# Kernel tuning notes

Measured on AMD Instinct MI355X. Metric: run time of the kernel, lower is better.

## Reference

```python
import jax, jax.numpy as jnp
import numpy as np

B = 32768

def _lin(x, w, b):
    return x @ w.T + b

def setup_inputs() -> dict:
    key = jax.random.key(0)
    ks = iter(jax.random.split(key, 40))
    def rn(shape, s=0.05):
        return jax.random.normal(next(ks), shape, dtype=jnp.float32) * s
    inp = {
        'img_feat': jax.random.normal(next(ks), (B, 256), dtype=jnp.float32),
        'instruction_idx': jax.random.randint(next(ks), (B, 1), 0, 4),
        '_hx': jax.random.normal(next(ks), (B, 256), dtype=jnp.float32),
        '_cx': jax.random.normal(next(ks), (B, 256), dtype=jnp.float32),
        'query': jax.random.normal(next(ks), (B, 256), dtype=jnp.float32),
        # parameters
        'emb': rn((4, 25), 1.0),
        'w_ta': rn((256, 25)), 'b_ta': rn((256,)),
        'w_ih': rn((1024, 512)), 'w_hh': rn((1024, 256)),
        'b_ih': rn((1024,)), 'b_hh': rn((1024,)),
        'w_q': rn((256, 256)), 'b_q': rn((256,)),
        'w_k': rn((256, 256)), 'b_k': rn((256,)),
        'w_ba': rn((512, 512)), 'b_ba': rn((512,)),
        'w_at': rn((256, 512)), 'b_at': rn((256,)),
        'w_p1': rn((128, 256)), 'b_p1': rn((128,)),
        'w_p2': rn((64, 128)), 'b_p2': rn((64,)),
        'w_p': rn((3, 64)), 'b_p': rn((3,)),
        'w_v1': rn((64, 256)), 'b_v1': rn((64,)),
        'w_v2': rn((32, 64)), 'b_v2': rn((32,)),
        'w_v': rn((1, 32)), 'b_v': rn((1,)),
    }
    return inp

def reference(img_feat, instruction_idx, _hx, _cx, query,
              emb, w_ta, b_ta, w_ih, w_hh, b_ih, b_hh,
              w_q, b_q, w_k, b_k, w_ba, b_ba, w_at, b_at,
              w_p1, b_p1, w_p2, b_p2, w_p, b_p,
              w_v1, b_v1, w_v2, b_v2, w_v, b_v):
    # embedding lookup [B,1,25] -> [B,25]
    we = emb[instruction_idx].reshape(instruction_idx.shape[0], -1)
    gated_att = jax.nn.sigmoid(_lin(we, w_ta, b_ta))          # [B,256]
    gated_fusion = img_feat * gated_att                        # [B,256]
    lstm_input = jnp.concatenate([gated_fusion, gated_att], 1) # [B,512]
    # LSTMCell (PyTorch gate order: i, f, g, o)
    gates = lstm_input @ w_ih.T + b_ih + _hx @ w_hh.T + b_hh   # [B,1024]
    i, f, g, o = jnp.split(gates, 4, axis=1)
    cx = jax.nn.sigmoid(f) * _cx + jax.nn.sigmoid(i) * jnp.tanh(g)
    hx = jax.nn.sigmoid(o) * jnp.tanh(cx)
    mlp_input = jnp.concatenate([gated_fusion, hx], 1)         # [B,512]
    mlp_attn = jax.nn.relu(_lin(mlp_input, w_ba, b_ba))        # [B,512]
    key_, val = jnp.split(mlp_attn, 2, axis=1)                 # [B,256] each
    w_q_out = jax.nn.relu(_lin(query, w_q, b_q))
    w_k_out = jax.nn.relu(_lin(key_, w_k, b_k))
    u_t = jnp.tanh(w_q_out + w_k_out)
    attention_vector = u_t * val
    attn_weight = jnp.concatenate([attention_vector, hx], 1)   # [B,512]
    attn_weight = jax.nn.relu(_lin(attn_weight, w_at, b_at))   # [B,256]
    pol = jax.nn.relu(_lin(attn_weight, w_p1, b_p1))
    pol = jax.nn.relu(_lin(pol, w_p2, b_p2))
    valh = jax.nn.relu(_lin(attn_weight, w_v1, b_v1))
    valh = jax.nn.relu(_lin(valh, w_v2, b_v2))
    return (_lin(valh, w_v, b_v), _lin(pol, w_p, b_p), hx, cx)
```

## Files before the change

### kernel.cpp

```cpp
#include <hip/hip_runtime.h>

typedef unsigned short u16;
typedef __bf16 bf16x8 __attribute__((ext_vector_type(8)));
typedef float f32x4 __attribute__((ext_vector_type(4)));
typedef u16 u16x8 __attribute__((ext_vector_type(8)));

#define TM 64
#define LDP 264
#define BTOT 32768

#define OFF_WIH 0
#define OFF_WHH 524288
#define OFF_WQ  786432
#define OFF_WK  851968
#define OFF_WBA 917504
#define OFF_WAT 1179648
#define OFF_WP1 1310720
#define OFF_WP2 1343488
#define OFF_WV1 1351680
#define OFF_WV2 1368064

__device__ __forceinline__ float b2f(u16 h) {
    union { unsigned int u; float f; } v; v.u = ((unsigned int)h) << 16; return v.f;
}
__device__ __forceinline__ u16 f2b(float f) {
    union { float f; unsigned int u; } v; v.f = f;
    unsigned int u = v.u + 0x7fffu + ((v.u >> 16) & 1u);
    return (u16)(u >> 16);
}
__device__ __forceinline__ float sigm(float x) { return 1.0f / (1.0f + __expf(-x)); }
__device__ __forceinline__ float tanhfast(float x) { return 1.0f - 2.0f / (__expf(2.0f * x) + 1.0f); }
__device__ __forceinline__ float relu(float x) { return x > 0.0f ? x : 0.0f; }
__device__ __forceinline__ bf16x8 ld8(const u16* p) { return *(const bf16x8*)p; }
__device__ __forceinline__ f32x4 mfma16(bf16x8 a, bf16x8 b, f32x4 c) {
    return __builtin_amdgcn_mfma_f32_16x16x32_bf16(a, b, c, 0, 0, 0);
}

__device__ __forceinline__ bool detect_f32(const void* imgp) {
    const unsigned int* w = (const unsigned int*)imgp;
    int hits = 0;
    #pragma unroll
    for (int i = 0; i < 16; ++i) {
        int e0 = (w[i] >> 7) & 0xFF;
        hits += (e0 >= 100 && e0 <= 140) ? 1 : 0;
    }
    return hits < 10;
}

__device__ __forceinline__ float ldin(const void* p, size_t i, bool f32) {
    return f32 ? ((const float*)p)[i] : b2f(((const u16*)p)[i]);
}
__device__ __forceinline__ void stout(void* o, size_t i, float v, bool f32) {
    if (f32) ((float*)o)[i] = v; else ((u16*)o)[i] = f2b(v);
}
__device__ __forceinline__ float ldin_nt(const void* p, size_t i, bool f32) {
    return f32 ? __builtin_nontemporal_load((const float*)p + i)
               : b2f(((const u16*)p)[i]);
}
__device__ __forceinline__ void stout_nt(void* o, size_t i, float v, bool f32) {
    if (f32) __builtin_nontemporal_store(v, (float*)o + i);
    else ((u16*)o)[i] = f2b(v);
}
__device__ __forceinline__ bf16x8 ldg8f_nt(const void* p, size_t i, bool f32) {
    u16 t[8];
    if (f32) {
        const f32x4* q = (const f32x4*)((const float*)p + i);
        f32x4 a = __builtin_nontemporal_load(q);
        f32x4 b = __builtin_nontemporal_load(q + 1);
        #pragma unroll
        for (int j = 0; j < 4; ++j) { t[j] = f2b(a[j]); t[4 + j] = f2b(b[j]); }
    } else {
        *(u16x8*)t = *(const u16x8*)((const u16*)p + i);
    }
    return *(bf16x8*)t;
}

struct CvtArgs {
    const void* src[10];
    unsigned int nchunk[10];
    unsigned int off8[10];
    unsigned int Kdim[10];
    const void* det;
};

__global__ __launch_bounds__(256) void cvt_weights(CvtArgs a, u16* ws) {
    const bool f32 = detect_f32(a.det);
    const int p = blockIdx.x;
    const void* s = a.src[p];
    const unsigned int K = a.Kdim[p];
    const unsigned int KK = K >> 5;
    const unsigned int msk = KK - 1u;
    const unsigned int sh = 31 - __clz((int)KK);
    const unsigned int n = a.nchunk[p];
    for (unsigned int g = blockIdx.y * blockDim.x + threadIdx.x; g < n;
         g += gridDim.y * blockDim.x) {
        const unsigned int lane = g & 63u;
        const unsigned int fi = g >> 6;
        const unsigned int kk = fi & msk;
        const unsigned int tn = fi >> sh;
        const unsigned int row = tn * 16u + (lane & 15u);
        const unsigned int col = kk * 32u + ((lane >> 4) << 3);
        const size_t si = (size_t)row * K + col;
        u16 t[8];
        if (f32) {
            const float* q = (const float*)s + si;
            #pragma unroll
            for (int j = 0; j < 8; ++j) t[j] = f2b(__builtin_nontemporal_load(q + j));
        } else {
            *(u16x8*)t = *(const u16x8*)((const u16*)s + si);
        }
        ((u16x8*)ws)[a.off8[p] + g] = *(u16x8*)t;
    }
}

__global__ __launch_bounds__(1024, 2) void ac_fused(
    const void* __restrict__ img, const int* __restrict__ insn,
    const void* __restrict__ hx_in, const void* __restrict__ cx_in,
    const void* __restrict__ query,
    const void* __restrict__ emb, const void* __restrict__ w_ta, const void* __restrict__ b_ta,
    const void* __restrict__ b_ih, const void* __restrict__ b_hh,
    const void* __restrict__ b_q, const void* __restrict__ b_k,
    const void* __restrict__ b_ba, const void* __restrict__ b_at,
    const void* __restrict__ b_p1, const void* __restrict__ b_p2,
    const void* __restrict__ w_p3, const void* __restrict__ b_p3,
    const void* __restrict__ b_v1, const void* __restrict__ b_v2,
    const void* __restrict__ w_v3, const void* __restrict__ b_v3,
    const u16* __restrict__ wsb, void* __restrict__ out)
{
    __shared__ __align__(16) u16 sGF[TM * LDP];
    __shared__ __align__(16) u16 sHX0[TM * LDP];
    __shared__ __align__(16) u16 sHX1[TM * LDP];
    __shared__ __align__(16) u16 sKEY[TM * LDP];
    __shared__ __align__(16) u16 sG[4 * LDP];
    __shared__ int sIDX[TM];

    const bool isf32 = detect_f32(img);
    const int tid  = threadIdx.x;
    const int lane = tid & 63;
    const int wv   = tid >> 6;
    const int l15  = lane & 15;
    const int quad = lane >> 4;
    const int q8   = quad * 8;
    const int ln8  = lane * 8;
    const int row0 = blockIdx.x * TM;

    if (tid < TM) sIDX[tid] = insn[row0 + tid];
    {
        int e = tid >> 8, n = tid & 255;
        float acc = ldin(b_ta, n, isf32);
        #pragma unroll
        for (int k = 0; k < 25; ++k)
            acc += ldin(emb, e * 25 + k, isf32) * ldin(w_ta, n * 25 + k, isf32);
        sG[e * LDP + n] = f2b(sigm(acc));
    }
    __syncthreads();

    for (int it = tid; it < TM * 32; it += 1024) {
        int r = it >> 5, c0 = (it & 31) << 3;
        int e = sIDX[r];
        u16x8 gv = *(const u16x8*)(sG + e * LDP + c0);
        float iv[8], hv[8];
        const size_t base = (size_t)(row0 + r) * 256 + c0;
        if (isf32) {
            const f32x4* ip = (const f32x4*)((const float*)img + base);
            const f32x4* hp = (const f32x4*)((const float*)hx_in + base);
            f32x4 a0 = __builtin_nontemporal_load(ip);
            f32x4 a1 = __builtin_nontemporal_load(ip + 1);
            f32x4 b0 = __builtin_nontemporal_load(hp);
            f32x4 b1 = __builtin_nontemporal_load(hp + 1);
            #pragma unroll
            for (int j = 0; j < 4; ++j) {
                iv[j] = a0[j]; iv[4 + j] = a1[j];
                hv[j] = b0[j]; hv[4 + j] = b1[j];
            }
        } else {
            u16x8 i8 = *(const u16x8*)((const u16*)img + base);
            u16x8 h8 = *(const u16x8*)((const u16*)hx_in + base);
            #pragma unroll
            for (int j = 0; j < 8; ++j) { iv[j] = b2f(i8[j]); hv[j] = b2f(h8[j]); }
        }
        u16x8 ov, hvv;
        #pragma unroll
        for (int j = 0; j < 8; ++j) {
            ov[j] = f2b(iv[j] * b2f(gv[j]));
            hvv[j] = f2b(hv[j]);
        }
        *(u16x8*)(sGF + r * LDP + c0) = ov;
        *(u16x8*)(sHX0 + r * LDP + c0) = hvv;
    }
    __syncthreads();

    {
        int eIdx[4];
        #pragma unroll
        for (int m = 0; m < 4; ++m) eIdx[m] = sIDX[m * 16 + l15];
        const u16* bih0 = wsb + OFF_WIH + ln8;
        const u16* bhh0 = wsb + OFF_WHH + ln8;
        const int c = wv;
        f32x4 acc[4][4] = {};
        #pragma unroll
        for (int kk = 0; kk < 8; ++kk) {
            bf16x8 a[4], b[4];
            #pragma unroll
            for (int m = 0; m < 4; ++m) a[m] = ld8(sGF + (m * 16 + l15) * LDP + kk * 32 + q8);
            #pragma unroll
            for (int g = 0; g < 4; ++g) b[g] = ld8(bih0 + (size_t)((g * 16 + c) * 16 + kk) * 512);
            #pragma unroll
            for (int g = 0; g < 4; ++g)
                #pragma unroll
                for (int m = 0; m < 4; ++m) acc[g][m] = mfma16(a[m], b[g], acc[g][m]);
        }
        #pragma unroll
        for (int kk = 0; kk < 8; ++kk) {
            bf16x8 a[4], b[4];
            #pragma unroll
            for (int m = 0; m < 4; ++m) a[m] = ld8(sG + eIdx[m] * LDP + kk * 32 + q8);
            #pragma unroll
            for (int g = 0; g < 4; ++g) b[g] = ld8(bih0 + (size_t)((g * 16 + c) * 16 + 8 + kk) * 512);
            #pragma unroll
            for (int g = 0; g < 4; ++g)
                #pragma unroll
                for (int m = 0; m < 4; ++m) acc[g][m] = mfma16(a[m], b[g], acc[g][m]);
        }
        #pragma unroll
        for (int kk = 0; kk < 8; ++kk) {
            bf16x8 a[4], b[4];
            #pragma unroll
            for (int m = 0; m < 4; ++m) a[m] = ld8(sHX0 + (m * 16 + l15) * LDP + kk * 32 + q8);
            #pragma unroll
            for (int g = 0; g < 4; ++g) b[g] = ld8(bhh0 + (size_t)((g * 16 + c) * 8 + kk) * 512);
            #pragma unroll
            for (int g = 0; g < 4; ++g)
                #pragma unroll
                for (int m = 0; m < 4; ++m) acc[g][m] = mfma16(a[m], b[g], acc[g][m]);
        }
        const int nc = c * 16 + l15;
        const float bi  = ldin(b_ih, nc, isf32)       + ldin(b_hh, nc, isf32);
        const float bff = ldin(b_ih, 256 + nc, isf32) + ldin(b_hh, 256 + nc, isf32);
        const float bg  = ldin(b_ih, 512 + nc, isf32) + ldin(b_hh, 512 + nc, isf32);
        const float bo  = ldin(b_ih, 768 + nc, isf32) + ldin(b_hh, 768 + nc, isf32);
        #pragma unroll
        for (int m = 0; m < 4; ++m) {
            #pragma unroll
            for (int r = 0; r < 4; ++r) {
                const int grow = m * 16 + quad * 4 + r;
                const size_t gidx = (size_t)(row0 + grow) * 256 + nc;
                const float cxo = ldin_nt(cx_in, gidx, isf32);
                const float iv = sigm(acc[0][m][r] + bi);
                const float fv = sigm(acc[1][m][r] + bff);
                const float gv = tanhfast(acc[2][m][r] + bg);
                const float ov = sigm(acc[3][m][r] + bo);
                const float cn = fv * cxo + iv * gv;
                const float hn = ov * tanhfast(cn);
                stout_nt(out, (size_t)(4 * BTOT) + gidx, hn, isf32);
                stout_nt(out, (size_t)(4 * BTOT) + (size_t)256 * BTOT + gidx, cn, isf32);
                sHX1[grow * LDP + nc] = f2b(hn);
            }
        }
    }
    __syncthreads();

    {
        f32x4 acc[2][4] = {};
        const u16* bb0 = wsb + OFF_WBA + ln8;
        #pragma unroll
        for (int kk = 0; kk < 8; ++kk) {
            bf16x8 a[4], b[2];
            #pragma unroll
            for (int m = 0; m < 4; ++m) a[m] = ld8(sGF + (m * 16 + l15) * LDP + kk * 32 + q8);
            #pragma unroll
            for (int t = 0; t < 2; ++t) b[t] = ld8(bb0 + (size_t)((wv * 2 + t) * 16 + kk) * 512);
            #pragma unroll
            for (int t = 0; t < 2; ++t)
                #pragma unroll
                for (int m = 0; m < 4; ++m) acc[t][m] = mfma16(a[m], b[t], acc[t][m]);
        }
        #pragma unroll
        for (int kk = 0; kk < 8; ++kk) {
            bf16x8 a[4], b[2];
            #pragma unroll
            for (int m = 0; m < 4; ++m) a[m] = ld8(sHX1 + (m * 16 + l15) * LDP + kk * 32 + q8);
            #pragma unroll
            for (int t = 0; t < 2; ++t) b[t] = ld8(bb0 + (size_t)((wv * 2 + t) * 16 + 8 + kk) * 512);
            #pragma unroll
            for (int t = 0; t < 2; ++t)
                #pragma unroll
                for (int m = 0; m < 4; ++m) acc[t][m] = mfma16(a[m], b[t], acc[t][m]);
        }
        #pragma unroll
        for (int t = 0; t < 2; ++t) {
            const int col = (wv * 2 + t) * 16 + l15;
            const float bb = ldin(b_ba, col, isf32);
            u16* dst = (col < 256) ? (sKEY + col) : (sHX0 + (col - 256));
            #pragma unroll
            for (int m = 0; m < 4; ++m)
                #pragma unroll
                for (int r = 0; r < 4; ++r)
                    dst[(m * 16 + quad * 4 + r) * LDP] = f2b(relu(acc[t][m][r] + bb));
        }
    }
    __syncthreads();

    {
        f32x4 cq[4] = {}, ck[4] = {};
        const u16* bq0 = wsb + OFF_WQ + ln8;
        const u16* bk0 = wsb + OFF_WK + ln8;
        #pragma unroll
        for (int kk = 0; kk < 8; ++kk) {
            bf16x8 aq[4], ak[4], bqf, bkf;
            #pragma unroll
            for (int m = 0; m < 4; ++m) {
                aq[m] = ldg8f_nt(query, (size_t)(row0 + m * 16 + l15) * 256 + kk * 32 + q8, isf32);
                ak[m] = ld8(sKEY + (m * 16 + l15) * LDP + kk * 32 + q8);
            }
            bqf = ld8(bq0 + (size_t)(wv * 8 + kk) * 512);
            bkf = ld8(bk0 + (size_t)(wv * 8 + kk) * 512);
            #pragma unroll
            for (int m = 0; m < 4; ++m) {
                cq[m] = mfma16(aq[m], bqf, cq[m]);
                ck[m] = mfma16(ak[m], bkf, ck[m]);
            }
        }
        const int col = wv * 16 + l15;
        const float bqv = ldin(b_q, col, isf32);
        const float bkv = ldin(b_k, col, isf32);
        #pragma unroll
        for (int m = 0; m < 4; ++m)
            #pragma unroll
            for (int r = 0; r < 4; ++r) {
                const int grow = m * 16 + quad * 4 + r;
                const float u = tanhfast(relu(cq[m][r] + bqv) + relu(ck[m][r] + bkv));
                sGF[grow * LDP + col] = f2b(u * b2f(sHX0[grow * LDP + col]));
            }
    }
    __syncthreads();

    {
        f32x4 acc[4] = {};
        const u16* bb0 = wsb + OFF_WAT + ln8;
        #pragma unroll
        for (int kk = 0; kk < 8; ++kk) {
            bf16x8 a[4], b;
            #pragma unroll
            for (int m = 0; m < 4; ++m) a[m] = ld8(sGF + (m * 16 + l15) * LDP + kk * 32 + q8);
            b = ld8(bb0 + (size_t)(wv * 16 + kk) * 512);
            #pragma unroll
            for (int m = 0; m < 4; ++m) acc[m] = mfma16(a[m], b, acc[m]);
        }
        #pragma unroll
        for (int kk = 0; kk < 8; ++kk) {
            bf16x8 a[4], b;
            #pragma unroll
            for (int m = 0; m < 4; ++m) a[m] = ld8(sHX1 + (m * 16 + l15) * LDP + kk * 32 + q8);
            b = ld8(bb0 + (size_t)(wv * 16 + 8 + kk) * 512);
            #pragma unroll
            for (int m = 0; m < 4; ++m) acc[m] = mfma16(a[m], b, acc[m]);
        }
        const int col = wv * 16 + l15;
        const float bb = ldin(b_at, col, isf32);
        #pragma unroll
        for (int m = 0; m < 4; ++m)
            #pragma unroll
            for (int r = 0; r < 4; ++r)
                sKEY[(m * 16 + quad * 4 + r) * LDP + col] = f2b(relu(acc[m][r] + bb));
    }
    __syncthreads();

    {
        const int m = wv & 3, half = wv >> 2;
        const int arow = m * 16 + l15;
        bf16x8 afr[8];
        #pragma unroll
        for (int kk = 0; kk < 8; ++kk) afr[kk] = ld8(sKEY + arow * LDP + kk * 32 + q8);
        {
            f32x4 acc[2] = {};
            #pragma unroll
            for (int kk = 0; kk < 8; ++kk)
                #pragma unroll
                for (int t = 0; t < 2; ++t)
                    acc[t] = mfma16(afr[kk], ld8(wsb + OFF_WP1 + (size_t)((half * 2 + t) * 8 + kk) * 512 + ln8), acc[t]);
            #pragma unroll
            for (int t = 0; t < 2; ++t) {
                const int col = (half * 2 + t) * 16 + l15;
                const float bb = ldin(b_p1, col, isf32);
                #pragma unroll
                for (int r = 0; r < 4; ++r)
                    sHX0[(m * 16 + quad * 4 + r) * LDP + col] = f2b(relu(acc[t][r] + bb));
            }
        }
        {
            f32x4 acc = {};
            #pragma unroll
            for (int kk = 0; kk < 8; ++kk)
                acc = mfma16(afr[kk], ld8(wsb + OFF_WV1 + (size_t)(half * 8 + kk) * 512 + ln8), acc);
            const int col = half * 16 + l15;
            const float bb = ldin(b_v1, col, isf32);
            #pragma unroll
            for (int r = 0; r < 4; ++r)
                sHX0[(m * 16 + quad * 4 + r) * LDP + 128 + col] = f2b(relu(acc[r] + bb));
        }
    }
    __syncthreads();

    {
        const int m = wv & 3, half = wv >> 2;
        const int arow = m * 16 + l15;
        const u16* a0 = sHX0 + arow * LDP;
        bf16x8 ap[4], av2[2];
        #pragma unroll
        for (int kk = 0; kk < 4; ++kk) ap[kk] = ld8(a0 + kk * 32 + q8);
        #pragma unroll
        for (int kk = 0; kk < 2; ++kk) av2[kk] = ld8(a0 + 128 + kk * 32 + q8);
        {
            f32x4 acc = {};
            #pragma unroll
            for (int kk = 0; kk < 4; ++kk)
                acc = mfma16(ap[kk], ld8(wsb + OFF_WP2 + (size_t)(half * 4 + kk) * 512 + ln8), acc);
            const int col = half * 16 + l15;
            const float bb = ldin(b_p2, col, isf32);
            #pragma unroll
            for (int r = 0; r < 4; ++r)
                sGF[(m * 16 + quad * 4 + r) * LDP + col] = f2b(relu(acc[r] + bb));
        }
        if (half < 2) {
            f32x4 acc = {};
            #pragma unroll
            for (int kk = 0; kk < 2; ++kk)
                acc = mfma16(av2[kk], ld8(wsb + OFF_WV2 + (size_t)(half * 2 + kk) * 512 + ln8), acc);
            const int col = half * 16 + l15;
            const float bb = ldin(b_v2, col, isf32);
            #pragma unroll
            for (int r = 0; r < 4; ++r)
                sGF[(m * 16 + quad * 4 + r) * LDP + 64 + col] = f2b(relu(acc[r] + bb));
        }
    }
    __syncthreads();

    if (tid < TM * 4) {
        const int r = tid >> 2, o = tid & 3;
        const int grow = row0 + r;
        const u16* rowp = sGF + r * LDP;
        if (o < 3) {
            float acc = ldin(b_p3, o, isf32);
            #pragma unroll
            for (int k = 0; k < 64; ++k) acc += b2f(rowp[k]) * ldin(w_p3, o * 64 + k, isf32);
            stout_nt(out, (size_t)BTOT + (size_t)grow * 3 + o, acc, isf32);
        } else {
            float acc = ldin(b_v3, 0, isf32);
            #pragma unroll
            for (int k = 0; k < 32; ++k) acc += b2f(rowp[64 + k]) * ldin(w_v3, k, isf32);
            stout_nt(out, (size_t)grow, acc, isf32);
        }
    }
}

extern "C" void kernel_launch(void* const* d_in, const int* in_sizes, int n_in,
                              void* d_out, int out_size, void* d_ws, size_t ws_size,
                              hipStream_t stream) {
    u16* ws = (u16*)d_ws;

    CvtArgs ca;
    const int srcIdx[10] = {8, 9, 12, 14, 16, 18, 20, 22, 26, 28};
    const unsigned int ns[10]   = {524288, 262144, 65536, 65536, 262144, 131072, 32768, 8192, 16384, 2048};
    const unsigned int off[10]  = {OFF_WIH, OFF_WHH, OFF_WQ, OFF_WK, OFF_WBA, OFF_WAT, OFF_WP1, OFF_WP2, OFF_WV1, OFF_WV2};
    const unsigned int kd[10]   = {512, 256, 256, 256, 512, 512, 256, 128, 256, 64};
    for (int i = 0; i < 10; ++i) {
        ca.src[i] = d_in[srcIdx[i]];
        ca.nchunk[i] = ns[i] / 8;
        ca.off8[i] = off[i] / 8;
        ca.Kdim[i] = kd[i];
    }
    ca.det = d_in[0];
    cvt_weights<<<dim3(10, 64), dim3(256), 0, stream>>>(ca, ws);

    ac_fused<<<dim3(BTOT / TM), dim3(1024), 0, stream>>>(
        d_in[0], (const int*)d_in[1], d_in[2], d_in[3], d_in[4],
        d_in[5], d_in[6], d_in[7],
        d_in[10], d_in[11],
        d_in[13], d_in[15],
        d_in[17], d_in[19],
        d_in[21], d_in[23],
        d_in[24], d_in[25],
        d_in[27], d_in[29],
        d_in[30], d_in[31],
        (const u16*)d_ws, d_out);
}
```

Before: 418.4 us.

## Swap MFMA operand order to vectorize epilogue global and LDS stores

Every MFMA now takes the weight fragment as the A operand and the activation as B. Each lane's four accumulator values then run along the output-feature dimension instead of the batch dimension. This lets the LSTM epilogue load cx and store hx/cx as 4-wide vectors, and lets all later epilogues write LDS as packed u16x4 stores instead of scattered scalar stores. The weight-conversion prep kernel also switches to two 16-byte nontemporal loads. In exchange, each lane now loads four bias values instead of one, and LDS write patterns change, which could alter bank conflicts.

```diff
diff --git a/kernel.cpp b/kernel.cpp
--- a/kernel.cpp
+++ b/kernel.cpp
@@ -4,6 +4,7 @@
 typedef __bf16 bf16x8 __attribute__((ext_vector_type(8)));
 typedef float f32x4 __attribute__((ext_vector_type(4)));
 typedef u16 u16x8 __attribute__((ext_vector_type(8)));
+typedef u16 u16x4 __attribute__((ext_vector_type(4)));
 
 #define TM 64
 #define LDP 264
@@ -50,16 +51,26 @@
 __device__ __forceinline__ float ldin(const void* p, size_t i, bool f32) {
     return f32 ? ((const float*)p)[i] : b2f(((const u16*)p)[i]);
 }
-__device__ __forceinline__ void stout(void* o, size_t i, float v, bool f32) {
-    if (f32) ((float*)o)[i] = v; else ((u16*)o)[i] = f2b(v);
-}
-__device__ __forceinline__ float ldin_nt(const void* p, size_t i, bool f32) {
-    return f32 ? __builtin_nontemporal_load((const float*)p + i)
-               : b2f(((const u16*)p)[i]);
-}
 __device__ __forceinline__ void stout_nt(void* o, size_t i, float v, bool f32) {
     if (f32) __builtin_nontemporal_store(v, (float*)o + i);
     else ((u16*)o)[i] = f2b(v);
+}
+__device__ __forceinline__ f32x4 ld4(const void* p, size_t i, bool f32) {
+    if (f32) return __builtin_nontemporal_load((const f32x4*)((const float*)p + i));
+    u16x4 q = *(const u16x4*)((const u16*)p + i);
+    f32x4 r;
+    #pragma unroll
+    for (int j = 0; j < 4; ++j) r[j] = b2f(q[j]);
+    return r;
+}
+__device__ __forceinline__ void st4(void* o, size_t i, f32x4 v, bool f32) {
+    if (f32) __builtin_nontemporal_store(v, (f32x4*)((float*)o + i));
+    else {
+        u16x4 p;
+        #pragma unroll
+        for (int j = 0; j < 4; ++j) p[j] = f2b(v[j]);
+        *(u16x4*)((u16*)o + i) = p;
+    }
 }
 __device__ __forceinline__ bf16x8 ldg8f_nt(const void* p, size_t i, bool f32) {
     u16 t[8];
@@ -103,9 +114,11 @@
         const size_t si = (size_t)row * K + col;
         u16 t[8];
         if (f32) {
-            const float* q = (const float*)s + si;
-            #pragma unroll
-            for (int j = 0; j < 8; ++j) t[j] = f2b(__builtin_nontemporal_load(q + j));
+            const f32x4* q = (const f32x4*)((const float*)s + si);
+            f32x4 va = __builtin_nontemporal_load(q);
+            f32x4 vb = __builtin_nontemporal_load(q + 1);
+            #pragma unroll
+            for (int j = 0; j < 4; ++j) { t[j] = f2b(va[j]); t[4 + j] = f2b(vb[j]); }
         } else {
             *(u16x8*)t = *(const u16x8*)((const u16*)s + si);
         }
@@ -141,6 +154,7 @@
     const int l15  = lane & 15;
     const int quad = lane >> 4;
     const int q8   = quad * 8;
+    const int q4   = quad * 4;
     const int ln8  = lane * 8;
     const int row0 = blockIdx.x * TM;
 
@@ -208,7 +222,7 @@
             #pragma unroll
             for (int g = 0; g < 4; ++g)
                 #pragma unroll
-                for (int m = 0; m < 4; ++m) acc[g][m] = mfma16(a[m], b[g], acc[g][m]);
+                for (int m = 0; m < 4; ++m) acc[g][m] = mfma16(b[g], a[m], acc[g][m]);
         }
         #pragma unroll
         for (int kk = 0; kk < 8; ++kk) {
@@ -220,7 +234,7 @@
             #pragma unroll
             for (int g = 0; g < 4; ++g)
                 #pragma unroll
-                for (int m = 0; m < 4; ++m) acc[g][m] = mfma16(a[m], b[g], acc[g][m]);
+                for (int m = 0; m < 4; ++m) acc[g][m] = mfma16(b[g], a[m], acc[g][m]);
         }
         #pragma unroll
         for (int kk = 0; kk < 8; ++kk) {
@@ -232,30 +246,36 @@
             #pragma unroll
             for (int g = 0; g < 4; ++g)
                 #pragma unroll
-                for (int m = 0; m < 4; ++m) acc[g][m] = mfma16(a[m], b[g], acc[g][m]);
-        }
-        const int nc = c * 16 + l15;
-        const float bi  = ldin(b_ih, nc, isf32)       + ldin(b_hh, nc, isf32);
-        const float bff = ldin(b_ih, 256 + nc, isf32) + ldin(b_hh, 256 + nc, isf32);
-        const float bg  = ldin(b_ih, 512 + nc, isf32) + ldin(b_hh, 512 + nc, isf32);
-        const float bo  = ldin(b_ih, 768 + nc, isf32) + ldin(b_hh, 768 + nc, isf32);
+                for (int m = 0; m < 4; ++m) acc[g][m] = mfma16(b[g], a[m], acc[g][m]);
+        }
+        const int nbase = c * 16 + q4;
+        float bI[4], bF[4], bG[4], bO[4];
+        #pragma unroll
+        for (int r = 0; r < 4; ++r) {
+            bI[r] = ldin(b_ih,       nbase + r, isf32) + ldin(b_hh,       nbase + r, isf32);
+            bF[r] = ldin(b_ih, 256 + nbase + r, isf32) + ldin(b_hh, 256 + nbase + r, isf32);
+            bG[r] = ldin(b_ih, 512 + nbase + r, isf32) + ldin(b_hh, 512 + nbase + r, isf32);
+            bO[r] = ldin(b_ih, 768 + nbase + r, isf32) + ldin(b_hh, 768 + nbase + r, isf32);
+        }
         #pragma unroll
         for (int m = 0; m < 4; ++m) {
+            const int batch = m * 16 + l15;
+            const size_t gbase = (size_t)(row0 + batch) * 256 + nbase;
+            f32x4 cxo = ld4(cx_in, gbase, isf32);
+            f32x4 hnv, cnv; u16x4 hpk;
             #pragma unroll
             for (int r = 0; r < 4; ++r) {
-                const int grow = m * 16 + quad * 4 + r;
-                const size_t gidx = (size_t)(row0 + grow) * 256 + nc;
-                const float cxo = ldin_nt(cx_in, gidx, isf32);
-                const float iv = sigm(acc[0][m][r] + bi);
-                const float fv = sigm(acc[1][m][r] + bff);
-                const float gv = tanhfast(acc[2][m][r] + bg);
-                const float ov = sigm(acc[3][m][r] + bo);
-                const float cn = fv * cxo + iv * gv;
+                const float iv = sigm(acc[0][m][r] + bI[r]);
+                const float fv = sigm(acc[1][m][r] + bF[r]);
+                const float gv = tanhfast(acc[2][m][r] + bG[r]);
+                const float ov = sigm(acc[3][m][r] + bO[r]);
+                const float cn = fv * cxo[r] + iv * gv;
                 const float hn = ov * tanhfast(cn);
-                stout_nt(out, (size_t)(4 * BTOT) + gidx, hn, isf32);
-                stout_nt(out, (size_t)(4 * BTOT) + (size_t)256 * BTOT + gidx, cn, isf32);
-                sHX1[grow * LDP + nc] = f2b(hn);
-            }
+                cnv[r] = cn; hnv[r] = hn; hpk[r] = f2b(hn);
+            }
+            st4(out, (size_t)(4 * BTOT) + gbase, hnv, isf32);
+            st4(out, (size_t)(4 * BTOT) + (size_t)256 * BTOT + gbase, cnv, isf32);
+            *(u16x4*)(sHX1 + batch * LDP + nbase) = hpk;
         }
     }
     __syncthreads();
@@ -273,7 +293,7 @@
             #pragma unroll
             for (int t = 0; t < 2; ++t)
                 #pragma unroll
-                for (int m = 0; m < 4; ++m) acc[t][m] = mfma16(a[m], b[t], acc[t][m]);
+                for (int m = 0; m < 4; ++m) acc[t][m] = mfma16(b[t], a[m], acc[t][m]);
         }
         #pragma unroll
         for (int kk = 0; kk < 8; ++kk) {
@@ -285,18 +305,22 @@
             #pragma unroll
             for (int t = 0; t < 2; ++t)
                 #pragma unroll
-                for (int m = 0; m < 4; ++m) acc[t][m] = mfma16(a[m], b[t], acc[t][m]);
+                for (int m = 0; m < 4; ++m) acc[t][m] = mfma16(b[t], a[m], acc[t][m]);
         }
         #pragma unroll
         for (int t = 0; t < 2; ++t) {
-            const int col = (wv * 2 + t) * 16 + l15;
-            const float bb = ldin(b_ba, col, isf32);
-            u16* dst = (col < 256) ? (sKEY + col) : (sHX0 + (col - 256));
-            #pragma unroll
-            for (int m = 0; m < 4; ++m)
-                #pragma unroll
-                for (int r = 0; r < 4; ++r)
-                    dst[(m * 16 + quad * 4 + r) * LDP] = f2b(relu(acc[t][m][r] + bb));
+            const int colb = (wv * 2 + t) * 16 + q4;
+            float bb[4];
+            #pragma unroll
+            for (int r = 0; r < 4; ++r) bb[r] = ldin(b_ba, colb + r, isf32);
+            u16* dst = (colb < 256) ? (sKEY + colb) : (sHX0 + (colb - 256));
+            #pragma unroll
+            for (int m = 0; m < 4; ++m) {
+                u16x4 pk;
+                #pragma unroll
+                for (int r = 0; r < 4; ++r) pk[r] = f2b(relu(acc[t][m][r] + bb[r]));
+                *(u16x4*)(dst + (m * 16 + l15) * LDP) = pk;
+            }
         }
     }
     __syncthreads();
@@ -317,21 +341,29 @@
             bkf = ld8(bk0 + (size_t)(wv * 8 + kk) * 512);
             #pragma unroll
             for (int m = 0; m < 4; ++m) {
-                cq[m] = mfma16(aq[m], bqf, cq[m]);
-                ck[m] = mfma16(ak[m], bkf, ck[m]);
-            }
-        }
-        const int col = wv * 16 + l15;
-        const float bqv = ldin(b_q, col, isf32);
-        const float bkv = ldin(b_k, col, isf32);
-        #pragma unroll
-        for (int m = 0; m < 4; ++m)
+                cq[m] = mfma16(bqf, aq[m], cq[m]);
+                ck[m] = mfma16(bkf, ak[m], ck[m]);
+            }
+        }
+        const int nbase = wv * 16 + q4;
+        float bqv[4], bkv[4];
+        #pragma unroll
+        for (int r = 0; r < 4; ++r) {
+            bqv[r] = ldin(b_q, nbase + r, isf32);
+            bkv[r] = ldin(b_k, nbase + r, isf32);
+        }
+        #pragma unroll
+        for (int m = 0; m < 4; ++m) {
+            const int batch = m * 16 + l15;
+            u16x4 vv = *(const u16x4*)(sHX0 + batch * LDP + nbase);
+            u16x4 pk;
             #pragma unroll
             for (int r = 0; r < 4; ++r) {
-                const int grow = m * 16 + quad * 4 + r;
-                const float u = tanhfast(relu(cq[m][r] + bqv) + relu(ck[m][r] + bkv));
-                sGF[grow * LDP + col] = f2b(u * b2f(sHX0[grow * LDP + col]));
-            }
+                const float u = tanhfast(relu(cq[m][r] + bqv[r]) + relu(ck[m][r] + bkv[r]));
+                pk[r] = f2b(u * b2f(vv[r]));
+            }
+            *(u16x4*)(sGF + batch * LDP + nbase) = pk;
+        }
     }
     __syncthreads();
 
@@ -345,7 +377,7 @@
             for (int m = 0; m < 4; ++m) a[m] = ld8(sGF + (m * 16 + l15) * LDP + kk * 32 + q8);
             b = ld8(bb0 + (size_t)(wv * 16 + kk) * 512);
             #pragma unroll
-            for (int m = 0; m < 4; ++m) acc[m] = mfma16(a[m], b, acc[m]);
+            for (int m = 0; m < 4; ++m) acc[m] = mfma16(b, a[m], acc[m]);
         }
         #pragma unroll
         for (int kk = 0; kk < 8; ++kk) {
@@ -354,58 +386,62 @@
             for (int m = 0; m < 4; ++m) a[m] = ld8(sHX1 + (m * 16 + l15) * LDP + kk * 32 + q8);
             b = ld8(bb0 + (size_t)(wv * 16 + 8 + kk) * 512);
             #pragma unroll
-            for (int m = 0; m < 4; ++m) acc[m] = mfma16(a[m], b, acc[m]);
-        }
-        const int col = wv * 16 + l15;
-        const float bb = ldin(b_at, col, isf32);
-        #pragma unroll
-        for (int m = 0; m < 4; ++m)
-            #pragma unroll
-            for (int r = 0; r < 4; ++r)
-                sKEY[(m * 16 + quad * 4 + r) * LDP + col] = f2b(relu(acc[m][r] + bb));
+            for (int m = 0; m < 4; ++m) acc[m] = mfma16(b, a[m], acc[m]);
+        }
+        const int nbase = wv * 16 + q4;
+        float bb[4];
+        #pragma unroll
+        for (int r = 0; r < 4; ++r) bb[r] = ldin(b_at, nbase + r, isf32);
+        #pragma unroll
+        for (int m = 0; m < 4; ++m) {
+            u16x4 pk;
+            #pragma unroll
+            for (int r = 0; r < 4; ++r) pk[r] = f2b(relu(acc[m][r] + bb[r]));
+            *(u16x4*)(sKEY + (m * 16 + l15) * LDP + nbase) = pk;
+        }
     }
     __syncthreads();
 
     {
         const int m = wv & 3, half = wv >> 2;
-        const int arow = m * 16 + l15;
+        const int batch = m * 16 + l15;
         bf16x8 afr[8];
         #pragma unroll
-        for (int kk = 0; kk < 8; ++kk) afr[kk] = ld8(sKEY + arow * LDP + kk * 32 + q8);
+        for (int kk = 0; kk < 8; ++kk) afr[kk] = ld8(sKEY + batch * LDP + kk * 32 + q8);
         {
             f32x4 acc[2] = {};
             #pragma unroll
             for (int kk = 0; kk < 8; ++kk)
                 #pragma unroll
                 for (int t = 0; t < 2; ++t)
-                    acc[t] = mfma16(afr[kk], ld8(wsb + OFF_WP1 + (size_t)((half * 2 + t) * 8 + kk) * 512 + ln8), acc[t]);
+                    acc[t] = mfma16(ld8(wsb + OFF_WP1 + (size_t)((half * 2 + t) * 8 + kk) * 512 + ln8), afr[kk], acc[t]);
             #pragma unroll
             for (int t = 0; t < 2; ++t) {
-                const int col = (half * 2 + t) * 16 + l15;
-                const float bb = ldin(b_p1, col, isf32);
-                #pragma unroll
-                for (int r = 0; r < 4; ++r)
-                    sHX0[(m * 16 + quad * 4 + r) * LDP + col] = f2b(relu(acc[t][r] + bb));
+                const int colb = (half * 2 + t) * 16 + q4;
+                u16x4 pk;
+                #pragma unroll
+                for (int r = 0; r < 4; ++r) pk[r] = f2b(relu(acc[t][r] + ldin(b_p1, colb + r, isf32)));
+                *(u16x4*)(sHX0 + batch * LDP + colb) = pk;
             }
         }
         {
             f32x4 acc = {};
             #pragma unroll
             for (int kk = 0; kk < 8; ++kk)
-                acc = mfma16(afr[kk], ld8(wsb + OFF_WV1 + (size_t)(half * 8 + kk) * 512 + ln8), acc);
-            const int col = half * 16 + l15;
-            const float bb = ldin(b_v1, col, isf32);
-            #pragma unroll
-            for (int r = 0; r < 4; ++r)
-                sHX0[(m * 16 + quad * 4 + r) * LDP + 128 + col] = f2b(relu(acc[r] + bb));
+                acc = mfma16(ld8(wsb + OFF_WV1 + (size_t)(half * 8 + kk) * 512 + ln8), afr[kk], acc);
+            const int colb = half * 16 + q4;
+            u16x4 pk;
+            #pragma unroll
+            for (int r = 0; r < 4; ++r) pk[r] = f2b(relu(acc[r] + ldin(b_v1, colb + r, isf32)));
+            *(u16x4*)(sHX0 + batch * LDP + 128 + colb) = pk;
         }
     }
     __syncthreads();
 
     {
         const int m = wv & 3, half = wv >> 2;
-        const int arow = m * 16 + l15;
-        const u16* a0 = sHX0 + arow * LDP;
+        const int batch = m * 16 + l15;
+        const u16* a0 = sHX0 + batch * LDP;
         bf16x8 ap[4], av2[2];
         #pragma unroll
         for (int kk = 0; kk < 4; ++kk) ap[kk] = ld8(a0 + kk * 32 + q8);
@@ -415,23 +451,23 @@
             f32x4 acc = {};
             #pragma unroll
             for (int kk = 0; kk < 4; ++kk)
-                acc = mfma16(ap[kk], ld8(wsb + OFF_WP2 + (size_t)(half * 4 + kk) * 512 + ln8), acc);
-            const int col = half * 16 + l15;
-            const float bb = ldin(b_p2, col, isf32);
-            #pragma unroll
-            for (int r = 0; r < 4; ++r)
-                sGF[(m * 16 + quad * 4 + r) * LDP + col] = f2b(relu(acc[r] + bb));
+                acc = mfma16(ld8(wsb + OFF_WP2 + (size_t)(half * 4 + kk) * 512 + ln8), ap[kk], acc);
+            const int colb = half * 16 + q4;
+            u16x4 pk;
+            #pragma unroll
+            for (int r = 0; r < 4; ++r) pk[r] = f2b(relu(acc[r] + ldin(b_p2, colb + r, isf32)));
+            *(u16x4*)(sGF + batch * LDP + colb) = pk;
         }
         if (half < 2) {
             f32x4 acc = {};
             #pragma unroll
             for (int kk = 0; kk < 2; ++kk)
-                acc = mfma16(av2[kk], ld8(wsb + OFF_WV2 + (size_t)(half * 2 + kk) * 512 + ln8), acc);
-            const int col = half * 16 + l15;
-            const float bb = ldin(b_v2, col, isf32);
-            #pragma unroll
-            for (int r = 0; r < 4; ++r)
-                sGF[(m * 16 + quad * 4 + r) * LDP + 64 + col] = f2b(relu(acc[r] + bb));
+                acc = mfma16(ld8(wsb + OFF_WV2 + (size_t)(half * 2 + kk) * 512 + ln8), av2[kk], acc);
+            const int colb = half * 16 + q4;
+            u16x4 pk;
+            #pragma unroll
+            for (int r = 0; r < 4; ++r) pk[r] = f2b(relu(acc[r] + ldin(b_v2, colb + r, isf32)));
+            *(u16x4*)(sGF + batch * LDP + 64 + colb) = pk;
         }
     }
     __syncthreads();
```

Result: no change. 421.9 us (+0.8%).
